# Performance work log

Hardware: AMD Instinct MI355X
Metric: run time of the kernel (lower is better)

The kernel has to match this reference:

```python
import jax, jax.numpy as jnp
import numpy as np

B = 64           # images
C = 100          # num_categories
LOOP = 3         # LOOP_NUM: max boxes per (image, category)
NB_PER = 150     # boxes per image
N = B * NB_PER   # total boxes
FEAT = 2052      # 2048 backbone feats + 4 bbox coords
OUT = 2048       # gcn_output_shape


def _occ_slots(key):
    """For each element, its occurrence index among equal-valued keys (stable order)."""
    n = key.shape[0]
    order = jnp.argsort(key, stable=True)
    sk = key[order]
    idx = jnp.arange(n)
    is_new = jnp.concatenate([jnp.ones((1,), bool), sk[1:] != sk[:-1]])
    run_start = jax.lax.cummax(jnp.where(is_new, idx, 0))
    pos = idx - run_start
    return jnp.zeros(n, dtype=jnp.int32).at[order].set(pos.astype(jnp.int32))


def setup_inputs() -> dict:
    key = jax.random.key(0)
    ks = jax.random.split(key, 8)
    image_features = jax.random.normal(ks[0], (N, 2048), jnp.float32)
    bbox_list = jax.random.uniform(ks[1], (N, 4), jnp.float32)
    global_features = jax.random.normal(ks[2], (B, C), jnp.float32)
    adj = jax.random.uniform(ks[3], (B, C, C), jnp.float32)
    X = jnp.full((C, C), 1e-6, jnp.float32)                 # nn.Parameter init
    lin_w = jax.random.normal(ks[4], (LOOP,), jnp.float32) * 0.5   # Linear(3,1) weight
    lin_b = jax.random.normal(ks[5], (), jnp.float32) * 0.1        # Linear(3,1) bias
    gc_w = jax.random.normal(ks[6], (FEAT, OUT), jnp.float32) / np.sqrt(FEAT)
    gc_b = jnp.zeros((OUT,), jnp.float32)
    # labels cycle 1..C so each (image, category) appears <= ceil(NB_PER/C)=2 <= LOOP times
    label_list = (jnp.arange(N, dtype=jnp.int32) % C) + 1
    batch = (jnp.arange(N, dtype=jnp.int32) // NB_PER)
    return dict(image_features=image_features, bbox_list=bbox_list,
                global_features=global_features, adj=adj, X=X,
                lin_w=lin_w, lin_b=lin_b, gc_w=gc_w, gc_b=gc_b,
                label_list=label_list, batch=batch)


def reference(image_features, bbox_list, global_features, adj, X,
              lin_w, lin_b, gc_w, gc_b, label_list, batch):
    # full_features = concat(backbone feats, bbox): [N, 2052]
    full = jnp.concatenate([image_features, bbox_list], axis=1)
    cat = label_list - 1
    # occurrence slot of each box within its (image, category) bucket
    slots = _occ_slots(batch.astype(jnp.int64) * C + cat.astype(jnp.int64))
    # scatter-build gcn_input: [B, C, LOOP, 2052]
    gcn_input = jnp.zeros((B, C, LOOP, FEAT), full.dtype).at[batch, cat, slots].set(full)
    # transpose(2,3) then Linear(LOOP -> 1) and squeeze: [B, C, 2052]
    x = jnp.einsum('bcld,l->bcd', gcn_input, lin_w) + lin_b
    # new_adj = X + adj; GraphConvolution: adj @ (x @ W) + b, then leaky_relu
    new_adj = X[None, :, :] + adj
    support = jnp.einsum('bcd,do->bco', x, gc_w)          # [B, C, 2048]
    gcn_out = jax.nn.leaky_relu(jnp.einsum('bcn,bno->bco', new_adj, support) + gc_b)
    # attention aggregate: [B,1,C] @ [B,C,OUT] -> [B,OUT]
    return jnp.einsum('bc,bco->bo', global_features, gcn_out)
```

## Files before the change

### kernel.cpp

```cpp
#include <hip/hip_runtime.h>
#include <stdint.h>

#define BB    64
#define CC    100
#define NBPER 150
#define NBOX  9600
#define FEAT  2052
#define KP    2112
#define NOUT  2048
#define MR    6400

typedef __attribute__((ext_vector_type(8))) short   short8;
typedef __attribute__((ext_vector_type(4))) float   floatx4;

__device__ __forceinline__ unsigned short f2bf(float f) {
  unsigned int u = __float_as_uint(f);
  u += 0x7FFFu + ((u >> 16) & 1u);
  return (unsigned short)(u >> 16);
}

__device__ __forceinline__ void async16(const void* g, void* l) {
  __builtin_amdgcn_global_load_lds((__attribute__((address_space(1))) void*)(g),
                                   (__attribute__((address_space(3))) void*)(l),
                                   16, 0, 0);
}

__global__ __launch_bounds__(256) void k_transpose(const float* __restrict__ gcw,
                                                   unsigned short* __restrict__ gcwT) {
  __shared__ float tile[32][33];
  const int ko = blockIdx.x;
  const int oo = blockIdx.y;
  const int tx = threadIdx.x, ty = threadIdx.y;
#pragma unroll
  for (int i = 0; i < 4; ++i) {
    const int k = ko * 32 + ty + i * 8;
    const int o = oo * 32 + tx;
    tile[ty + i * 8][tx] = (k < FEAT) ? gcw[(size_t)k * NOUT + o] : 0.f;
  }
  __syncthreads();
#pragma unroll
  for (int i = 0; i < 4; ++i) {
    const int o = oo * 32 + ty + i * 8;
    const int k = ko * 32 + tx;
    gcwT[(size_t)o * KP + k] = f2bf(tile[tx][ty + i * 8]);
  }
}

__global__ __launch_bounds__(256) void k_bucket(const int* __restrict__ labels,
                                                int* __restrict__ boxidx) {
  __shared__ int lab[NBPER];
  const int b = blockIdx.x, tid = threadIdx.x;
  if (tid < NBPER) lab[tid] = labels[b * NBPER + tid];
  __syncthreads();
  if (tid < CC) {
    int cnt = 0;
    int out[3] = {-1, -1, -1};
    for (int i = 0; i < NBPER; ++i) {
      if (lab[i] == tid + 1 && cnt < 3) { out[cnt] = b * NBPER + i; ++cnt; }
    }
    const int base = (b * CC + tid) * 3;
    boxidx[base] = out[0]; boxidx[base + 1] = out[1]; boxidx[base + 2] = out[2];
  }
}

__global__ __launch_bounds__(256) void k_buildx(const float* __restrict__ imgf,
                                                const float* __restrict__ bbox,
                                                const float* __restrict__ lw,
                                                const float* __restrict__ lb,
                                                const int* __restrict__ boxidx,
                                                unsigned short* __restrict__ xbf) {
  const int c = blockIdx.x, b = blockIdx.y;
  const int r = b * CC + c;
  const int base = r * 3;
  const int i0 = boxidx[base], i1 = boxidx[base + 1], i2 = boxidx[base + 2];
  const float w0 = lw[0], w1 = lw[1], w2 = lw[2], bias = lb[0];
  for (int s = threadIdx.x; s < KP / 8; s += 256) {
    const int d0 = s * 8;
    float v[8];
#pragma unroll
    for (int q = 0; q < 8; ++q) v[q] = 0.f;
    if (d0 < 2048) {
      if (i0 >= 0) {
        const float4* p = (const float4*)(imgf + (size_t)i0 * 2048 + d0);
        float4 u0 = p[0], u1 = p[1];
        v[0] += w0 * u0.x; v[1] += w0 * u0.y; v[2] += w0 * u0.z; v[3] += w0 * u0.w;
        v[4] += w0 * u1.x; v[5] += w0 * u1.y; v[6] += w0 * u1.z; v[7] += w0 * u1.w;
      }
      if (i1 >= 0) {
        const float4* p = (const float4*)(imgf + (size_t)i1 * 2048 + d0);
        float4 u0 = p[0], u1 = p[1];
        v[0] += w1 * u0.x; v[1] += w1 * u0.y; v[2] += w1 * u0.z; v[3] += w1 * u0.w;
        v[4] += w1 * u1.x; v[5] += w1 * u1.y; v[6] += w1 * u1.z; v[7] += w1 * u1.w;
      }
      if (i2 >= 0) {
        const float4* p = (const float4*)(imgf + (size_t)i2 * 2048 + d0);
        float4 u0 = p[0], u1 = p[1];
        v[0] += w2 * u0.x; v[1] += w2 * u0.y; v[2] += w2 * u0.z; v[3] += w2 * u0.w;
        v[4] += w2 * u1.x; v[5] += w2 * u1.y; v[6] += w2 * u1.z; v[7] += w2 * u1.w;
      }
#pragma unroll
      for (int q = 0; q < 8; ++q) v[q] += bias;
    } else if (d0 == 2048) {
      if (i0 >= 0) { float4 u = *(const float4*)(bbox + (size_t)i0 * 4);
        v[0] += w0 * u.x; v[1] += w0 * u.y; v[2] += w0 * u.z; v[3] += w0 * u.w; }
      if (i1 >= 0) { float4 u = *(const float4*)(bbox + (size_t)i1 * 4);
        v[0] += w1 * u.x; v[1] += w1 * u.y; v[2] += w1 * u.z; v[3] += w1 * u.w; }
      if (i2 >= 0) { float4 u = *(const float4*)(bbox + (size_t)i2 * 4);
        v[0] += w2 * u.x; v[1] += w2 * u.y; v[2] += w2 * u.z; v[3] += w2 * u.w; }
      v[0] += bias; v[1] += bias; v[2] += bias; v[3] += bias;
    }
    unsigned short o[8] __attribute__((aligned(16)));
#pragma unroll
    for (int q = 0; q < 8; ++q) o[q] = f2bf(v[q]);
    *(uint4*)(xbf + (size_t)r * KP + d0) = *(const uint4*)o;
  }
}

__global__ __launch_bounds__(256) void k_gemm1(const unsigned short* __restrict__ A,
                                               const unsigned short* __restrict__ Bt,
                                               unsigned short* __restrict__ Cb) {
  __shared__ unsigned short Asm[128 * 64] __attribute__((aligned(16)));
  __shared__ unsigned short Bsm[128 * 64] __attribute__((aligned(16)));
  const int tid  = threadIdx.x;
  const int lane = tid & 63;
  const int w    = tid >> 6;
  const int m0   = blockIdx.y * 128;
  const int n0   = blockIdx.x * 128;
  const int wm   = (w & 1) * 64;
  const int wn   = (w >> 1) * 64;
  const int srow = lane >> 3;
  const int gk   = (((lane & 7) - srow) & 7) * 8;
  const int quad = lane >> 4;
  const int lrow = lane & 15;
  const int rot  = (lane & 7) * 8;

  floatx4 acc[4][4] = {};

  for (int kb = 0; kb < KP / 64; ++kb) {
    const int k0 = kb * 64;
#pragma unroll
    for (int t = 0; t < 4; ++t) {
      const int chunk = t * 4 + w;
      const int row = chunk * 8 + srow;
      async16(A  + (size_t)(m0 + row) * KP + (k0 + gk), &Asm[chunk * 512]);
      async16(Bt + (size_t)(n0 + row) * KP + (k0 + gk), &Bsm[chunk * 512]);
    }
    __syncthreads();
#pragma unroll
    for (int kp = 0; kp < 2; ++kp) {
      const int koff = (kp * 32 + quad * 8 + rot) & 63;
      short8 af[4], bfr[4];
#pragma unroll
      for (int i = 0; i < 4; ++i)
        af[i]  = *(const short8*)&Asm[(wm + i * 16 + lrow) * 64 + koff];
#pragma unroll
      for (int j = 0; j < 4; ++j)
        bfr[j] = *(const short8*)&Bsm[(wn + j * 16 + lrow) * 64 + koff];
#pragma unroll
      for (int i = 0; i < 4; ++i)
#pragma unroll
        for (int j = 0; j < 4; ++j)
          acc[i][j] = __builtin_amdgcn_mfma_f32_16x16x32_bf16(af[i], bfr[j], acc[i][j], 0, 0, 0);
    }
    __syncthreads();
  }
#pragma unroll
  for (int i = 0; i < 4; ++i)
#pragma unroll
    for (int j = 0; j < 4; ++j) {
      const int col = n0 + wn + j * 16 + lrow;
#pragma unroll
      for (int rr = 0; rr < 4; ++rr) {
        const int row = m0 + wm + i * 16 + quad * 4 + rr;
        Cb[(size_t)row * NOUT + col] = f2bf(acc[i][j][rr]);
      }
    }
}

__global__ __launch_bounds__(256) void k_gemm2(const float* __restrict__ X,
                                               const float* __restrict__ adj,
                                               const unsigned short* __restrict__ S,
                                               const float* __restrict__ gf,
                                               const float* __restrict__ gcb,
                                               float* __restrict__ outp) {
  __shared__ unsigned int A2w[128 * 64] __attribute__((aligned(16)));
  __shared__ unsigned int Ssw[128 * 64] __attribute__((aligned(16)));
  __shared__ float gsm[128];
  const int tid = threadIdx.x;
  const int o0  = blockIdx.x * 128;
  const int b   = blockIdx.y;

  if (tid < 128) gsm[tid] = (tid < CC) ? gf[b * CC + tid] : 0.f;

#pragma unroll
  for (int it = 0; it < 32; ++it) {
    const int idx = it * 256 + tid;
    const int c = idx >> 6, j = idx & 63;
    unsigned int v = 0;
    if (c < CC && j < 50) {
      const float2 a2 = *(const float2*)(adj + (size_t)b * (CC * CC) + c * CC + 2 * j);
      const float2 x2 = *(const float2*)(X + c * CC + 2 * j);
      v = (unsigned int)f2bf(a2.x + x2.x) | ((unsigned int)f2bf(a2.y + x2.y) << 16);
    }
    A2w[c * 64 + ((j + 4 * (c & 15)) & 63)] = v;
  }
#pragma unroll
  for (int it = 0; it < 32; ++it) {
    const int idx = it * 256 + tid;
    const int o = idx & 127, np = idx >> 7;
    unsigned int v = 0;
    const int n0 = 2 * np;
    if (n0 < CC) {
      unsigned int lo = S[(size_t)(b * CC + n0) * NOUT + o0 + o];
      unsigned int hi = (n0 + 1 < CC) ? (unsigned int)S[(size_t)(b * CC + n0 + 1) * NOUT + o0 + o] : 0u;
      v = lo | (hi << 16);
    }
    Ssw[o * 64 + ((np + 4 * (o & 15)) & 63)] = v;
  }
  __syncthreads();

  const int lane = tid & 63;
  const int w    = tid >> 6;
  const int wm   = (w & 1) * 64;
  const int wn   = (w >> 1) * 64;
  const int quad = lane >> 4;
  const int lrow = lane & 15;

  floatx4 acc[4][4] = {};
#pragma unroll
  for (int kp = 0; kp < 4; ++kp) {
    const int kw = (kp * 16 + quad * 4 + 4 * lrow) & 63;
    short8 af[4], bfr[4];
#pragma unroll
    for (int i = 0; i < 4; ++i)
      af[i] = *(const short8*)&A2w[(wm + i * 16 + lrow) * 64 + kw];
#pragma unroll
    for (int j = 0; j < 4; ++j)
      bfr[j] = *(const short8*)&Ssw[(wn + j * 16 + lrow) * 64 + kw];
#pragma unroll
    for (int i = 0; i < 4; ++i)
#pragma unroll
      for (int j = 0; j < 4; ++j)
        acc[i][j] = __builtin_amdgcn_mfma_f32_16x16x32_bf16(af[i], bfr[j], acc[i][j], 0, 0, 0);
  }
  __syncthreads();

  float* red = (float*)A2w;
  const int slot = (w & 1) * 4 + quad;
#pragma unroll
  for (int j = 0; j < 4; ++j) {
    const int ol = wn + j * 16 + lrow;
    const float bias = gcb[o0 + ol];
    float s = 0.f;
#pragma unroll
    for (int i = 0; i < 4; ++i) {
#pragma unroll
      for (int rr = 0; rr < 4; ++rr) {
        const int c = wm + i * 16 + quad * 4 + rr;
        float t = acc[i][j][rr] + bias;
        t = (t > 0.f) ? t : 0.01f * t;
        s += gsm[c] * t;
      }
    }
    red[ol * 9 + slot] = s;
  }
  __syncthreads();
  if (tid < 128) {
    float s = 0.f;
#pragma unroll
    for (int t = 0; t < 8; ++t) s += red[tid * 9 + t];
    outp[(size_t)b * NOUT + o0 + tid] = s;
  }
}

extern "C" void kernel_launch(void* const* d_in, const int* in_sizes, int n_in,
                              void* d_out, int out_size, void* d_ws, size_t ws_size,
                              hipStream_t stream) {
  const float* imgf   = (const float*)d_in[0];
  const float* bbox   = (const float*)d_in[1];
  const float* gfeat  = (const float*)d_in[2];
  const float* adj    = (const float*)d_in[3];
  const float* X      = (const float*)d_in[4];
  const float* lw     = (const float*)d_in[5];
  const float* lb     = (const float*)d_in[6];
  const float* gcw    = (const float*)d_in[7];
  const float* gcb    = (const float*)d_in[8];
  const int*   labels = (const int*)d_in[9];

  char* ws = (char*)d_ws;
  int*            boxidx   = (int*)(ws);
  unsigned short* xbf      = (unsigned short*)(ws + 76800);
  unsigned short* gcwT     = (unsigned short*)(ws + 27110400);
  unsigned short* supportB = (unsigned short*)(ws + 35761152);
  float*          outp     = (float*)d_out;

  k_transpose<<<dim3(KP / 32, NOUT / 32), dim3(32, 8), 0, stream>>>(gcw, gcwT);
  k_bucket<<<dim3(BB), dim3(256), 0, stream>>>(labels, boxidx);
  k_buildx<<<dim3(CC, BB), dim3(256), 0, stream>>>(imgf, bbox, lw, lb, boxidx, xbf);
  k_gemm1<<<dim3(NOUT / 128, MR / 128), dim3(256), 0, stream>>>(xbf, gcwT, supportB);
  k_gemm2<<<dim3(NOUT / 128, BB), dim3(256), 0, stream>>>(X, adj, supportB, gfeat, gcb, outp);
}
```

Before: 296.4 us.

## Fuse bucketing into buildx, prefetch gemm1 tiles, transpose support for gemm2

```diff
diff --git a/kernel.cpp b/kernel.cpp
--- a/kernel.cpp
+++ b/kernel.cpp
@@ -4,7 +4,6 @@
 #define BB    64
 #define CC    100
 #define NBPER 150
-#define NBOX  9600
 #define FEAT  2052
 #define KP    2112
 #define NOUT  2048
@@ -46,35 +45,28 @@
   }
 }
 
-__global__ __launch_bounds__(256) void k_bucket(const int* __restrict__ labels,
-                                                int* __restrict__ boxidx) {
-  __shared__ int lab[NBPER];
-  const int b = blockIdx.x, tid = threadIdx.x;
-  if (tid < NBPER) lab[tid] = labels[b * NBPER + tid];
-  __syncthreads();
-  if (tid < CC) {
-    int cnt = 0;
-    int out[3] = {-1, -1, -1};
-    for (int i = 0; i < NBPER; ++i) {
-      if (lab[i] == tid + 1 && cnt < 3) { out[cnt] = b * NBPER + i; ++cnt; }
-    }
-    const int base = (b * CC + tid) * 3;
-    boxidx[base] = out[0]; boxidx[base + 1] = out[1]; boxidx[base + 2] = out[2];
-  }
-}
-
 __global__ __launch_bounds__(256) void k_buildx(const float* __restrict__ imgf,
                                                 const float* __restrict__ bbox,
                                                 const float* __restrict__ lw,
                                                 const float* __restrict__ lb,
-                                                const int* __restrict__ boxidx,
+                                                const int* __restrict__ labels,
                                                 unsigned short* __restrict__ xbf) {
+  __shared__ int lab[NBPER];
+  __shared__ int sidx[3];
   const int c = blockIdx.x, b = blockIdx.y;
+  const int tid = threadIdx.x;
+  if (tid < NBPER) lab[tid] = labels[b * NBPER + tid];
+  __syncthreads();
+  if (tid == 0) {
+    int cnt = 0; sidx[0] = -1; sidx[1] = -1; sidx[2] = -1;
+    for (int i = 0; i < NBPER; ++i)
+      if (lab[i] == c + 1 && cnt < 3) { sidx[cnt] = b * NBPER + i; ++cnt; }
+  }
+  __syncthreads();
   const int r = b * CC + c;
-  const int base = r * 3;
-  const int i0 = boxidx[base], i1 = boxidx[base + 1], i2 = boxidx[base + 2];
+  const int i0 = sidx[0], i1 = sidx[1], i2 = sidx[2];
   const float w0 = lw[0], w1 = lw[1], w2 = lw[2], bias = lb[0];
-  for (int s = threadIdx.x; s < KP / 8; s += 256) {
+  for (int s = tid; s < KP / 8; s += 256) {
     const int d0 = s * 8;
     float v[8];
 #pragma unroll
@@ -124,8 +116,11 @@
   const int tid  = threadIdx.x;
   const int lane = tid & 63;
   const int w    = tid >> 6;
-  const int m0   = blockIdx.y * 128;
-  const int n0   = blockIdx.x * 128;
+  const int v    = blockIdx.y * gridDim.x + blockIdx.x;
+  const int ncol = (v & 7) * 2 + ((v >> 3) & 1);
+  const int mrow = v >> 4;
+  const int m0   = mrow * 128;
+  const int n0   = ncol * 128;
   const int wm   = (w & 1) * 64;
   const int wn   = (w >> 1) * 64;
   const int srow = lane >> 3;
@@ -134,18 +129,38 @@
   const int lrow = lane & 15;
   const int rot  = (lane & 7) * 8;
 
+  size_t aoff[4], boff[4];
+  int ldsoff[4];
+#pragma unroll
+  for (int t = 0; t < 4; ++t) {
+    const int chunk = t * 4 + w;
+    const int row = chunk * 8 + srow;
+    aoff[t] = (size_t)(m0 + row) * KP + gk;
+    boff[t] = (size_t)(n0 + row) * KP + gk;
+    ldsoff[t] = chunk * 512 + lane * 8;
+  }
+
   floatx4 acc[4][4] = {};
 
+#pragma unroll
+  for (int t = 0; t < 4; ++t) {
+    const int chunk = t * 4 + w;
+    async16(A  + aoff[t], &Asm[chunk * 512]);
+    async16(Bt + boff[t], &Bsm[chunk * 512]);
+  }
+  __syncthreads();
+
+  uint4 pa[4], pb[4];
   for (int kb = 0; kb < KP / 64; ++kb) {
-    const int k0 = kb * 64;
-#pragma unroll
-    for (int t = 0; t < 4; ++t) {
-      const int chunk = t * 4 + w;
-      const int row = chunk * 8 + srow;
-      async16(A  + (size_t)(m0 + row) * KP + (k0 + gk), &Asm[chunk * 512]);
-      async16(Bt + (size_t)(n0 + row) * KP + (k0 + gk), &Bsm[chunk * 512]);
-    }
-    __syncthreads();
+    const bool more = (kb + 1) < (KP / 64);
+    if (more) {
+      const int knext = (kb + 1) * 64;
+#pragma unroll
+      for (int t = 0; t < 4; ++t) {
+        pa[t] = *(const uint4*)(A  + aoff[t] + knext);
+        pb[t] = *(const uint4*)(Bt + boff[t] + knext);
+      }
+    }
 #pragma unroll
     for (int kp = 0; kp < 2; ++kp) {
       const int koff = (kp * 32 + quad * 8 + rot) & 63;
@@ -163,6 +178,14 @@
           acc[i][j] = __builtin_amdgcn_mfma_f32_16x16x32_bf16(af[i], bfr[j], acc[i][j], 0, 0, 0);
     }
     __syncthreads();
+    if (more) {
+#pragma unroll
+      for (int t = 0; t < 4; ++t) {
+        *(uint4*)&Asm[ldsoff[t]] = pa[t];
+        *(uint4*)&Bsm[ldsoff[t]] = pb[t];
+      }
+      __syncthreads();
+    }
   }
 #pragma unroll
   for (int i = 0; i < 4; ++i)
@@ -177,75 +200,99 @@
     }
 }
 
+__global__ __launch_bounds__(256) void k_str(const unsigned short* __restrict__ SB,
+                                             unsigned short* __restrict__ ST) {
+  __shared__ unsigned short t[32][33];
+  const int o0 = blockIdx.x * 32;
+  const int r0 = blockIdx.y * 32;
+  const int tx = threadIdx.x & 31, ty = threadIdx.x >> 5;
+#pragma unroll
+  for (int i = 0; i < 4; ++i)
+    t[ty + i * 8][tx] = SB[(size_t)(r0 + ty + i * 8) * NOUT + o0 + tx];
+  __syncthreads();
+#pragma unroll
+  for (int i = 0; i < 4; ++i) {
+    const int o = o0 + ty + i * 8;
+    const int r = r0 + tx;
+    const int b = r / 100;
+    const int c = r - b * 100;
+    ST[((size_t)b * NOUT + o) * 128 + c] = t[tx][ty + i * 8];
+  }
+}
+
 __global__ __launch_bounds__(256) void k_gemm2(const float* __restrict__ X,
                                                const float* __restrict__ adj,
-                                               const unsigned short* __restrict__ S,
+                                               const unsigned short* __restrict__ ST,
                                                const float* __restrict__ gf,
                                                const float* __restrict__ gcb,
                                                float* __restrict__ outp) {
-  __shared__ unsigned int A2w[128 * 64] __attribute__((aligned(16)));
-  __shared__ unsigned int Ssw[128 * 64] __attribute__((aligned(16)));
+  __shared__ unsigned short A2s[128 * 64] __attribute__((aligned(16)));
+  __shared__ unsigned short Ssm[128 * 64] __attribute__((aligned(16)));
   __shared__ float gsm[128];
+  __shared__ float red[128 * 9];
   const int tid = threadIdx.x;
   const int o0  = blockIdx.x * 128;
   const int b   = blockIdx.y;
-
   if (tid < 128) gsm[tid] = (tid < CC) ? gf[b * CC + tid] : 0.f;
-
-#pragma unroll
-  for (int it = 0; it < 32; ++it) {
-    const int idx = it * 256 + tid;
-    const int c = idx >> 6, j = idx & 63;
-    unsigned int v = 0;
-    if (c < CC && j < 50) {
-      const float2 a2 = *(const float2*)(adj + (size_t)b * (CC * CC) + c * CC + 2 * j);
-      const float2 x2 = *(const float2*)(X + c * CC + 2 * j);
-      v = (unsigned int)f2bf(a2.x + x2.x) | ((unsigned int)f2bf(a2.y + x2.y) << 16);
-    }
-    A2w[c * 64 + ((j + 4 * (c & 15)) & 63)] = v;
-  }
-#pragma unroll
-  for (int it = 0; it < 32; ++it) {
-    const int idx = it * 256 + tid;
-    const int o = idx & 127, np = idx >> 7;
-    unsigned int v = 0;
-    const int n0 = 2 * np;
-    if (n0 < CC) {
-      unsigned int lo = S[(size_t)(b * CC + n0) * NOUT + o0 + o];
-      unsigned int hi = (n0 + 1 < CC) ? (unsigned int)S[(size_t)(b * CC + n0 + 1) * NOUT + o0 + o] : 0u;
-      v = lo | (hi << 16);
-    }
-    Ssw[o * 64 + ((np + 4 * (o & 15)) & 63)] = v;
-  }
-  __syncthreads();
 
   const int lane = tid & 63;
   const int w    = tid >> 6;
+  const int srow = lane >> 3;
+  const int gk   = (((lane & 7) - srow) & 7) * 8;
+  const int quad = lane >> 4;
+  const int lrow = lane & 15;
+  const int rot  = (lane & 7) * 8;
   const int wm   = (w & 1) * 64;
   const int wn   = (w >> 1) * 64;
-  const int quad = lane >> 4;
-  const int lrow = lane & 15;
 
   floatx4 acc[4][4] = {};
-#pragma unroll
-  for (int kp = 0; kp < 4; ++kp) {
-    const int kw = (kp * 16 + quad * 4 + 4 * lrow) & 63;
-    short8 af[4], bfr[4];
-#pragma unroll
-    for (int i = 0; i < 4; ++i)
-      af[i] = *(const short8*)&A2w[(wm + i * 16 + lrow) * 64 + kw];
-#pragma unroll
-    for (int j = 0; j < 4; ++j)
-      bfr[j] = *(const short8*)&Ssw[(wn + j * 16 + lrow) * 64 + kw];
-#pragma unroll
-    for (int i = 0; i < 4; ++i)
+
+  for (int kb = 0; kb < 2; ++kb) {
+    const int k0 = kb * 64;
+    __syncthreads();
+#pragma unroll
+    for (int t = 0; t < 4; ++t) {
+      const int chunk = t * 4 + w;
+      const int orow = chunk * 8 + srow;
+      async16(ST + ((size_t)b * NOUT + o0 + orow) * 128 + k0 + gk, &Ssm[chunk * 512]);
+    }
+    {
+      const int ngrp = tid & 15;
+      const int cb   = tid >> 4;
+      const int n    = k0 + ngrp * 4;
+#pragma unroll
+      for (int it = 0; it < 8; ++it) {
+        const int c = it * 16 + cb;
+        unsigned short pk[4] __attribute__((aligned(8))) = {0, 0, 0, 0};
+        if (c < CC && n < CC) {
+          const float4 a4 = *(const float4*)(adj + (size_t)b * (CC * CC) + c * CC + n);
+          const float4 x4 = *(const float4*)(X + c * CC + n);
+          pk[0] = f2bf(a4.x + x4.x); pk[1] = f2bf(a4.y + x4.y);
+          pk[2] = f2bf(a4.z + x4.z); pk[3] = f2bf(a4.w + x4.w);
+        }
+        *(uint2*)&A2s[c * 64 + ((ngrp * 4 + 8 * (c & 7)) & 63)] = *(const uint2*)pk;
+      }
+    }
+    __syncthreads();
+#pragma unroll
+    for (int kp = 0; kp < 2; ++kp) {
+      const int koff = (kp * 32 + quad * 8 + rot) & 63;
+      short8 af[4], bfr[4];
+#pragma unroll
+      for (int i = 0; i < 4; ++i)
+        af[i]  = *(const short8*)&A2s[(wm + i * 16 + lrow) * 64 + koff];
 #pragma unroll
       for (int j = 0; j < 4; ++j)
-        acc[i][j] = __builtin_amdgcn_mfma_f32_16x16x32_bf16(af[i], bfr[j], acc[i][j], 0, 0, 0);
-  }
-  __syncthreads();
-
-  float* red = (float*)A2w;
+        bfr[j] = *(const short8*)&Ssm[(wn + j * 16 + lrow) * 64 + koff];
+#pragma unroll
+      for (int i = 0; i < 4; ++i)
+#pragma unroll
+        for (int j = 0; j < 4; ++j)
+          acc[i][j] = __builtin_amdgcn_mfma_f32_16x16x32_bf16(af[i], bfr[j], acc[i][j], 0, 0, 0);
+    }
+  }
+  __syncthreads();
+
   const int slot = (w & 1) * 4 + quad;
 #pragma unroll
   for (int j = 0; j < 4; ++j) {
@@ -288,15 +335,15 @@
   const int*   labels = (const int*)d_in[9];
 
   char* ws = (char*)d_ws;
-  int*            boxidx   = (int*)(ws);
-  unsigned short* xbf      = (unsigned short*)(ws + 76800);
-  unsigned short* gcwT     = (unsigned short*)(ws + 27110400);
-  unsigned short* supportB = (unsigned short*)(ws + 35761152);
+  unsigned short* xbf      = (unsigned short*)(ws);
+  unsigned short* gcwT     = (unsigned short*)(ws + 27033600);
+  unsigned short* supportB = (unsigned short*)(ws + 35684352);
+  unsigned short* supportT = (unsigned short*)(ws);
   float*          outp     = (float*)d_out;
 
   k_transpose<<<dim3(KP / 32, NOUT / 32), dim3(32, 8), 0, stream>>>(gcw, gcwT);
-  k_bucket<<<dim3(BB), dim3(256), 0, stream>>>(labels, boxidx);
-  k_buildx<<<dim3(CC, BB), dim3(256), 0, stream>>>(imgf, bbox, lw, lb, boxidx, xbf);
-  k_gemm1<<<dim3(NOUT / 128, MR / 128), dim3(256), 0, stream>>>(xbf, gcwT, supportB);
-  k_gemm2<<<dim3(NOUT / 128, BB), dim3(256), 0, stream>>>(X, adj, supportB, gfeat, gcb, outp);
-}
+  k_buildx<<<dim3(CC, BB), dim3(256), 0, stream>>>(imgf, bbox, lw, lb, labels, xbf);
+  k_gemm1<<<dim3(16, 50), dim3(256), 0, stream>>>(xbf, gcwT, supportB);
+  k_str<<<dim3(NOUT / 32, MR / 32), dim3(256), 0, stream>>>(supportB, supportT);
+  k_gemm2<<<dim3(NOUT / 128, BB), dim3(256), 0, stream>>>(X, adj, supportT, gfeat, gcb, outp);
+}
```

New measurement: 504.1 us. 70.1% more time.
